# Kernel tuning notes

Measured on AMD Instinct MI355X. Metric: run time of the kernel, lower is better.

Reference implementation:

```python
import jax, jax.numpy as jnp
import numpy as np

N = 8192
HID = 64
TAU = 0.8
LAMBDA = 0.5
POS_DENSITY = 0.005


def setup_inputs() -> dict:
    key = jax.random.key(0)
    k1, k2, k3, k4, k5, k6, k7 = jax.random.split(key, 7)
    x1 = jax.random.normal(k1, (N, HID), dtype=jnp.float32)
    x2 = jax.random.normal(k2, (N, HID), dtype=jnp.float32)
    # xavier_uniform with gain=1.414 for square [HID, HID] linears
    limit = 1.414 * np.sqrt(6.0 / (HID + HID))
    W1 = jax.random.uniform(k3, (HID, HID), dtype=jnp.float32, minval=-limit, maxval=limit)
    b1 = jnp.zeros((HID,), dtype=jnp.float32)
    W2 = jax.random.uniform(k4, (HID, HID), dtype=jnp.float32, minval=-limit, maxval=limit)
    b2 = jnp.zeros((HID,), dtype=jnp.float32)
    pm = (jax.random.uniform(k5, (N, N), dtype=jnp.float32) < POS_DENSITY).astype(jnp.float32)
    positive_matrix = jnp.maximum(pm, jnp.eye(N, dtype=jnp.float32))
    return {"x1": x1, "x2": x2, "W1": W1, "b1": b1, "W2": W2, "b2": b2,
            "positive_matrix": positive_matrix}


def _project(x, W1, b1, W2, b2):
    # nn.Linear(hidden, hidden) -> ELU -> nn.Linear(hidden, hidden)
    h = jax.nn.elu(x @ W1.T + b1)
    return h @ W2.T + b2


def _l2norm(z, eps=1e-12):
    # F.normalize(p=2, dim=1): x / max(||x||, eps)
    n = jnp.linalg.norm(z, axis=-1, keepdims=True)
    return z / jnp.maximum(n, eps)


def _sim(z1, z2, tau):
    return jnp.exp((_l2norm(z1) @ _l2norm(z2).T) / tau)  # [N, N]


def _masked_loss(sim_mat, pos):
    row = sim_mat / (jnp.sum(sim_mat, axis=-1, keepdims=True) + 1e-8)
    return -jnp.log(jnp.sum(row * pos, axis=-1) + 1e-8).mean()


def reference(x1, x2, W1, b1, W2, b2, positive_matrix):
    z1 = _project(x1, W1, b1, W2, b2)
    z2 = _project(x2, W1, b1, W2, b2)
    sc_mp = _sim(z1, z2, TAU)
    mp_sc = _sim(z2, z1, TAU)
    sc_loss = _masked_loss(sc_mp, positive_matrix)
    mp_loss = _masked_loss(mp_sc, positive_matrix)
    return sc_loss * LAMBDA + mp_loss * (1.0 - LAMBDA)
```

## Files before the change

kernel.cpp:

```cpp
#include <hip/hip_runtime.h>
#include <hip/hip_bf16.h>

#define N 8192
#define HID 64
#define JC 8

typedef __attribute__((ext_vector_type(4))) float f32x4;
typedef __attribute__((ext_vector_type(8))) __bf16 bf16x8;

__device__ __forceinline__ void gload_lds16(const float* g, float* l) {
  __builtin_amdgcn_global_load_lds(
      (const __attribute__((address_space(1))) void*)g,
      (__attribute__((address_space(3))) void*)l, 16, 0, 0);
}

__global__ __launch_bounds__(256) void proj_kernel(
    const float* __restrict__ x1, const float* __restrict__ x2,
    const float* __restrict__ W1, const float* __restrict__ b1,
    const float* __restrict__ W2, const float* __restrict__ b2,
    __bf16* __restrict__ Z1h, __bf16* __restrict__ Z2h,
    float* __restrict__ stats)
{
  __shared__ __align__(16) float w1s[64*68];
  __shared__ __align__(16) float w2s[64*68];
  __shared__ __align__(16) float xs[4][64];
  __shared__ __align__(16) float hs[4][64];

  const int tid  = threadIdx.x;
  const int lane = tid & 63;
  const int w    = tid >> 6;

  int gtid = blockIdx.x * 256 + tid;
  if (gtid < 4*N) stats[gtid] = 0.f;

  for (int idx = tid; idx < 64*64; idx += 256) {
    int j = idx >> 6, k = idx & 63;
    w1s[j*68+k] = W1[idx];
    w2s[j*68+k] = W2[idx];
  }
  __syncthreads();

  const float bias1 = b1[lane];
  const float bias2 = b2[lane];

  const int wave_global = blockIdx.x * 4 + w;
  #pragma unroll 1
  for (int it = 0; it < 4; ++it) {
    int R = wave_global * 4 + it;
    const float* src; __bf16* dst;
    if (R < N) { src = x1 + (size_t)R*HID;      dst = Z1h + (size_t)R*HID; }
    else       { src = x2 + (size_t)(R-N)*HID;  dst = Z2h + (size_t)(R-N)*HID; }

    float xv = src[lane];
    xs[w][lane] = xv;
    float acc = bias1;
    #pragma unroll
    for (int qq = 0; qq < 16; ++qq) {
      f32x4 xq = *(const f32x4*)&xs[w][qq*4];
      f32x4 wq = *(const f32x4*)&w1s[lane*68 + qq*4];
      acc += xq.x*wq.x + xq.y*wq.y + xq.z*wq.z + xq.w*wq.w;
    }
    float h = acc > 0.f ? acc : expm1f(acc);
    hs[w][lane] = h;
    float acc2 = bias2;
    #pragma unroll
    for (int qq = 0; qq < 16; ++qq) {
      f32x4 hq = *(const f32x4*)&hs[w][qq*4];
      f32x4 wq = *(const f32x4*)&w2s[lane*68 + qq*4];
      acc2 += hq.x*wq.x + hq.y*wq.y + hq.z*wq.z + hq.w*wq.w;
    }
    float z = acc2;
    float ss = z*z;
    #pragma unroll
    for (int m = 1; m < 64; m <<= 1) ss += __shfl_xor(ss, m);
    float inv = 1.0f / fmaxf(sqrtf(ss), 1e-12f);
    dst[lane] = (__bf16)(z * inv);
  }
}

__global__ __launch_bounds__(256) void sim_kernel(
    const __bf16* __restrict__ Z1h, const __bf16* __restrict__ Z2h,
    const float* __restrict__ pos,
    float* __restrict__ rowsum1, float* __restrict__ num1,
    float* __restrict__ rowsum2, float* __restrict__ num2)
{
  __shared__ __align__(16) float pbuf[2][64][64];

  const int tid  = threadIdx.x;
  const int lane = tid & 63;
  const int w    = tid >> 6;
  const int r16  = lane & 15;
  const int q    = lane >> 4;

  const int bi  = blockIdx.x / JC;
  const int jc  = blockIdx.x % JC;
  const int i0b = bi*64;
  const int i0  = i0b + w*16;

  const __bf16* z1r = Z1h + (size_t)(i0 + r16)*HID + q*8;
  const __bf16* z2r = Z2h + (size_t)(i0 + r16)*HID + q*8;
  const bf16x8 a1lo = *(const bf16x8*)(z1r);
  const bf16x8 a1hi = *(const bf16x8*)(z1r + 32);
  const bf16x8 a2lo = *(const bf16x8*)(z2r);
  const bf16x8 a2hi = *(const bf16x8*)(z2r + 32);

  float s1 = 0.f, n1 = 0.f, s2 = 0.f, n2 = 0.f;

  const int jbeg = jc * (N/JC);
  const float Cexp = 1.8033688011112042f;

#define STAGE(BUF, JJ) { \
    _Pragma("unroll") \
    for (int rr = 0; rr < 4; ++rr) { \
      int row_t = w*16 + rr*4 + (lane >> 4); \
      int slot  = lane & 15; \
      const float* gsrc = pos + (size_t)(i0b + row_t)*N + (JJ) + (((slot ^ (row_t & 7))) << 2); \
      gload_lds16(gsrc, &pbuf[BUF][w*16 + rr*4][0]); \
    } }

  STAGE(0, jbeg)

  int cur = 0;
  #pragma unroll 1
  for (int ss = 0; ss < 16; ++ss) {
    const int jj = jbeg + ss*64;
    if (ss != 15) {
      STAGE(cur ^ 1, jj + 64)
      asm volatile("s_waitcnt vmcnt(4)" ::: "memory");
    } else {
      asm volatile("s_waitcnt vmcnt(0)" ::: "memory");
    }
    __builtin_amdgcn_sched_barrier(0);

    #pragma unroll
    for (int cc = 0; cc < 64; cc += 32) {
      const int j0 = jj + cc;
      bf16x8 b2l[2], b2h[2], b1l[2], b1h[2];
      f32x4 pv[2];
      #pragma unroll
      for (int c = 0; c < 2; ++c) {
        const __bf16* zj2 = Z2h + (size_t)(j0 + c*16 + r16)*HID + q*8;
        const __bf16* zj1 = Z1h + (size_t)(j0 + c*16 + r16)*HID + q*8;
        b2l[c] = *(const bf16x8*)(zj2);
        b2h[c] = *(const bf16x8*)(zj2 + 32);
        b1l[c] = *(const bf16x8*)(zj1);
        b1h[c] = *(const bf16x8*)(zj1 + 32);
        int g = (cc >> 2) + c*4 + q;
        int s = g ^ (r16 & 7);
        pv[c] = *(const f32x4*)&pbuf[cur][w*16 + r16][s*4];
      }
      #pragma unroll
      for (int c = 0; c < 2; ++c) {
        f32x4 zero4 = {0.f,0.f,0.f,0.f};
        f32x4 d1 = __builtin_amdgcn_mfma_f32_16x16x32_bf16(b2l[c], a1lo, zero4, 0,0,0);
        d1       = __builtin_amdgcn_mfma_f32_16x16x32_bf16(b2h[c], a1hi, d1,    0,0,0);
        f32x4 d2 = __builtin_amdgcn_mfma_f32_16x16x32_bf16(b1l[c], a2lo, zero4, 0,0,0);
        d2       = __builtin_amdgcn_mfma_f32_16x16x32_bf16(b1h[c], a2hi, d2,    0,0,0);
        #pragma unroll
        for (int r = 0; r < 4; ++r) {
          float e1 = exp2f(d1[r] * Cexp);
          float e2 = exp2f(d2[r] * Cexp);
          s1 += e1; n1 += e1 * pv[c][r];
          s2 += e2; n2 += e2 * pv[c][r];
        }
      }
    }
    cur ^= 1;
  }
#undef STAGE

  s1 += __shfl_xor(s1, 16); s1 += __shfl_xor(s1, 32);
  n1 += __shfl_xor(n1, 16); n1 += __shfl_xor(n1, 32);
  s2 += __shfl_xor(s2, 16); s2 += __shfl_xor(s2, 32);
  n2 += __shfl_xor(n2, 16); n2 += __shfl_xor(n2, 32);

  if (lane < 16) {
    int row = i0 + r16;
    atomicAdd(&rowsum1[row], s1);
    atomicAdd(&num1[row],    n1);
    atomicAdd(&rowsum2[row], s2);
    atomicAdd(&num2[row],    n2);
  }
}

__global__ __launch_bounds__(1024) void loss_kernel(
    const float* __restrict__ rowsum1, const float* __restrict__ num1,
    const float* __restrict__ rowsum2, const float* __restrict__ num2,
    float* __restrict__ out)
{
  __shared__ float part[16];
  const int tid = threadIdx.x, lane = tid & 63, w = tid >> 6;
  float acc = 0.f;
  for (int i = tid; i < N; i += 1024) {
    float sc = -logf(num1[i]/(rowsum1[i]+1e-8f) + 1e-8f);
    float mp = -logf(num2[i]/(rowsum2[i]+1e-8f) + 1e-8f);
    acc += 0.5f*sc + 0.5f*mp;
  }
  #pragma unroll
  for (int m = 1; m < 64; m <<= 1) acc += __shfl_xor(acc, m);
  if (lane == 0) part[w] = acc;
  __syncthreads();
  if (tid == 0) {
    float t = 0.f;
    #pragma unroll
    for (int k = 0; k < 16; ++k) t += part[k];
    out[0] = t * (1.0f/N);
  }
}

extern "C" void kernel_launch(void* const* d_in, const int* in_sizes, int n_in,
                              void* d_out, int out_size, void* d_ws, size_t ws_size,
                              hipStream_t stream) {
  const float* x1  = (const float*)d_in[0];
  const float* x2  = (const float*)d_in[1];
  const float* W1  = (const float*)d_in[2];
  const float* b1  = (const float*)d_in[3];
  const float* W2  = (const float*)d_in[4];
  const float* b2  = (const float*)d_in[5];
  const float* pos = (const float*)d_in[6];

  char* ws = (char*)d_ws;
  __bf16* Z1h = (__bf16*)ws;
  __bf16* Z2h = (__bf16*)(ws + (size_t)N*HID*sizeof(__bf16));
  size_t zbytes = (size_t)2*N*HID*sizeof(__bf16);
  float* rowsum1 = (float*)(ws + zbytes);
  float* num1    = rowsum1 + N;
  float* rowsum2 = num1 + N;
  float* num2    = rowsum2 + N;

  proj_kernel<<<1024, 256, 0, stream>>>(x1, x2, W1, b1, W2, b2, Z1h, Z2h, rowsum1);
  sim_kernel<<<128*JC, 256, 0, stream>>>(Z1h, Z2h, pos, rowsum1, num1, rowsum2, num2);
  loss_kernel<<<1, 1024, 0, stream>>>(rowsum1, num1, rowsum2, num2, (float*)d_out);
}
```

Baseline: 438.2 us.

## Software-pipeline Z-tile loads with register double-buffering in sim kernel

Restructures the sim kernel main loop so the bf16 Z tiles for the next 32-column half-chunk are loaded into a second register set while the current set feeds the MFMAs and exps. Explicit vmcnt waits are retuned to track the interleaved Z loads and LDS staging of the positive-mask tile. The aim is to hide global/L2 latency of the Z reads, which were previously issued and consumed back-to-back. The cost is higher register pressure from two full sets of B operands, and correctness now depends on hand-counted outstanding-load counts.

```diff
diff --git a/kernel.cpp b/kernel.cpp
--- a/kernel.cpp
+++ b/kernel.cpp
@@ -13,6 +13,8 @@
       (const __attribute__((address_space(1))) void*)g,
       (__attribute__((address_space(3))) void*)l, 16, 0, 0);
 }
+
+#define FENCE asm volatile("" ::: "memory")
 
 __global__ __launch_bounds__(256) void proj_kernel(
     const float* __restrict__ x1, const float* __restrict__ x2,
@@ -109,6 +111,9 @@
   const int jbeg = jc * (N/JC);
   const float Cexp = 1.8033688011112042f;
 
+  bf16x8 Ab2l0, Ab2h0, Ab1l0, Ab1h0, Ab2l1, Ab2h1, Ab1l1, Ab1h1;
+  bf16x8 Bb2l0, Bb2h0, Bb1l0, Bb1h0, Bb2l1, Bb2h1, Bb1l1, Bb1h1;
+
 #define STAGE(BUF, JJ) { \
     _Pragma("unroll") \
     for (int rr = 0; rr < 4; ++rr) { \
@@ -118,56 +123,71 @@
       gload_lds16(gsrc, &pbuf[BUF][w*16 + rr*4][0]); \
     } }
 
+#define LOADZ(P, J0) { \
+    const __bf16* zj2a = Z2h + (size_t)((J0) + r16)*HID + q*8; \
+    const __bf16* zj1a = Z1h + (size_t)((J0) + r16)*HID + q*8; \
+    const __bf16* zj2b = Z2h + (size_t)((J0) + 16 + r16)*HID + q*8; \
+    const __bf16* zj1b = Z1h + (size_t)((J0) + 16 + r16)*HID + q*8; \
+    P##b2l0 = *(const bf16x8*)(zj2a); P##b2h0 = *(const bf16x8*)(zj2a + 32); \
+    P##b1l0 = *(const bf16x8*)(zj1a); P##b1h0 = *(const bf16x8*)(zj1a + 32); \
+    P##b2l1 = *(const bf16x8*)(zj2b); P##b2h1 = *(const bf16x8*)(zj2b + 32); \
+    P##b1l1 = *(const bf16x8*)(zj1b); P##b1h1 = *(const bf16x8*)(zj1b + 32); \
+  }
+
+#define COMPC(P, C, CC) { \
+    int g = ((CC) >> 2) + (C)*4 + q; \
+    int s = g ^ (r16 & 7); \
+    f32x4 pv = *(const f32x4*)&pbuf[buf][w*16 + r16][s*4]; \
+    f32x4 zero4 = {0.f,0.f,0.f,0.f}; \
+    f32x4 d1 = __builtin_amdgcn_mfma_f32_16x16x32_bf16(P##b2l##C, a1lo, zero4, 0,0,0); \
+    d1       = __builtin_amdgcn_mfma_f32_16x16x32_bf16(P##b2h##C, a1hi, d1,    0,0,0); \
+    f32x4 d2 = __builtin_amdgcn_mfma_f32_16x16x32_bf16(P##b1l##C, a2lo, zero4, 0,0,0); \
+    d2       = __builtin_amdgcn_mfma_f32_16x16x32_bf16(P##b1h##C, a2hi, d2,    0,0,0); \
+    _Pragma("unroll") \
+    for (int r = 0; r < 4; ++r) { \
+      float e1 = exp2f(d1[r] * Cexp); \
+      float e2 = exp2f(d2[r] * Cexp); \
+      s1 += e1; n1 += e1 * pv[r]; \
+      s2 += e2; n2 += e2 * pv[r]; \
+    } }
+
+#define COMPUTE(P, CC) { COMPC(P, 0, CC) COMPC(P, 1, CC) }
+
+  int buf = 0;
   STAGE(0, jbeg)
-
-  int cur = 0;
+  FENCE;
+  LOADZ(A, jbeg)
+  FENCE;
+
   #pragma unroll 1
-  for (int ss = 0; ss < 16; ++ss) {
-    const int jj = jbeg + ss*64;
-    if (ss != 15) {
-      STAGE(cur ^ 1, jj + 64)
-      asm volatile("s_waitcnt vmcnt(4)" ::: "memory");
-    } else {
-      asm volatile("s_waitcnt vmcnt(0)" ::: "memory");
-    }
-    __builtin_amdgcn_sched_barrier(0);
-
-    #pragma unroll
-    for (int cc = 0; cc < 64; cc += 32) {
-      const int j0 = jj + cc;
-      bf16x8 b2l[2], b2h[2], b1l[2], b1h[2];
-      f32x4 pv[2];
-      #pragma unroll
-      for (int c = 0; c < 2; ++c) {
-        const __bf16* zj2 = Z2h + (size_t)(j0 + c*16 + r16)*HID + q*8;
-        const __bf16* zj1 = Z1h + (size_t)(j0 + c*16 + r16)*HID + q*8;
-        b2l[c] = *(const bf16x8*)(zj2);
-        b2h[c] = *(const bf16x8*)(zj2 + 32);
-        b1l[c] = *(const bf16x8*)(zj1);
-        b1h[c] = *(const bf16x8*)(zj1 + 32);
-        int g = (cc >> 2) + c*4 + q;
-        int s = g ^ (r16 & 7);
-        pv[c] = *(const f32x4*)&pbuf[cur][w*16 + r16][s*4];
-      }
-      #pragma unroll
-      for (int c = 0; c < 2; ++c) {
-        f32x4 zero4 = {0.f,0.f,0.f,0.f};
-        f32x4 d1 = __builtin_amdgcn_mfma_f32_16x16x32_bf16(b2l[c], a1lo, zero4, 0,0,0);
-        d1       = __builtin_amdgcn_mfma_f32_16x16x32_bf16(b2h[c], a1hi, d1,    0,0,0);
-        f32x4 d2 = __builtin_amdgcn_mfma_f32_16x16x32_bf16(b1l[c], a2lo, zero4, 0,0,0);
-        d2       = __builtin_amdgcn_mfma_f32_16x16x32_bf16(b1h[c], a2hi, d2,    0,0,0);
-        #pragma unroll
-        for (int r = 0; r < 4; ++r) {
-          float e1 = exp2f(d1[r] * Cexp);
-          float e2 = exp2f(d2[r] * Cexp);
-          s1 += e1; n1 += e1 * pv[c][r];
-          s2 += e2; n2 += e2 * pv[c][r];
-        }
-      }
-    }
-    cur ^= 1;
+  for (int t = 0; t < 15; ++t) {
+    const int jj = jbeg + t*64;
+    LOADZ(B, jj + 32)
+    FENCE;
+    STAGE(buf ^ 1, jj + 64)
+    FENCE;
+    asm volatile("s_waitcnt vmcnt(12)" ::: "memory");
+    COMPUTE(A, 0)
+    FENCE;
+    LOADZ(A, jj + 64)
+    FENCE;
+    asm volatile("s_waitcnt vmcnt(12)" ::: "memory");
+    COMPUTE(B, 32)
+    buf ^= 1;
+  }
+  {
+    const int jj = jbeg + 15*64;
+    LOADZ(B, jj + 32)
+    FENCE;
+    asm volatile("s_waitcnt vmcnt(8)" ::: "memory");
+    COMPUTE(A, 0)
+    asm volatile("s_waitcnt vmcnt(0)" ::: "memory");
+    COMPUTE(B, 32)
   }
 #undef STAGE
+#undef LOADZ
+#undef COMPC
+#undef COMPUTE
 
   s1 += __shfl_xor(s1, 16); s1 += __shfl_xor(s1, 32);
   n1 += __shfl_xor(n1, 16); n1 += __shfl_xor(n1, 32);
```

Measured after the change: 441.8 us. No clear change (+0.8%).
